# Kernel tuning notes

Measured on AMD Instinct MI355X. Metric: run time of the kernel, lower is better.

Reference implementation:

```python
import jax, jax.numpy as jnp
import numpy as np

NEG_SLOPE = 0.2
EPS = 1e-16


def setup_inputs() -> dict:
    key = jax.random.key(0)
    k1, k2, k3, k4 = jax.random.split(key, 4)
    N, H, F, E = 50000, 4, 32, 800000
    nodes_features = jax.random.normal(k1, (N, H, F), dtype=jnp.float32)
    edge_index = jax.random.randint(k2, (2, E), 0, N, dtype=jnp.int64)
    scoring_fn_source = jax.random.normal(k3, (1, H, F), dtype=jnp.float32)
    scoring_fn_target = jax.random.normal(k4, (1, H, F), dtype=jnp.float32)
    return {
        "nodes_features": nodes_features,
        "scoring_fn_source": scoring_fn_source,
        "scoring_fn_target": scoring_fn_target,
        "edge_index": edge_index,
    }


def reference(nodes_features, scoring_fn_source, scoring_fn_target, edge_index):
    # nodes_features: [N, H, F]; edge_index: [2, E] with row 0 = target, row 1 = source
    num_of_nodes = nodes_features.shape[0]
    trg = edge_index[0]
    src = edge_index[1]

    # Per-node attention logits per head: [N, H]
    scores_source = (nodes_features * scoring_fn_source).sum(axis=-1)
    scores_target = (nodes_features * scoring_fn_target).sum(axis=-1)

    # Lift N -> E via gather: [E, H]
    scores_lifted = scores_source[src] + scores_target[trg]
    src_nodes_features_lifted = nodes_features[src]  # [E, H, F]

    scores_per_edge = jax.nn.leaky_relu(scores_lifted, NEG_SLOPE)
    # Global max subtraction for numerical stability (matches original code)
    scores_per_edge = scores_per_edge - scores_per_edge.max()
    exp_scores = jnp.exp(scores_per_edge)

    # Segment softmax denominator via scatter-add, then gather back per edge
    neighborhood_sums = jax.ops.segment_sum(exp_scores, trg, num_segments=num_of_nodes)
    denom = neighborhood_sums[trg]  # [E, H]

    attentions_per_edge = (exp_scores / (denom + EPS))[..., None]  # [E, H, 1]
    return attentions_per_edge, src_nodes_features_lifted
```

## Files before the change

kernel.cpp:

```cpp
#include <hip/hip_runtime.h>

#define NEG_SLOPE 0.2f
#define EPSV 1e-16f

typedef float f32x4 __attribute__((ext_vector_type(4)));

__device__ __forceinline__ unsigned fenc(float f) {
    unsigned b = __float_as_uint(f);
    return b ^ ((b & 0x80000000u) ? 0xFFFFFFFFu : 0x80000000u);
}
__device__ __forceinline__ float fdec(unsigned u) {
    unsigned b = (u & 0x80000000u) ? (u ^ 0x80000000u) : ~u;
    return __uint_as_float(b);
}
#define FENC_NEG_INF 0x007FFFFFu

__global__ void detect_idx_kernel(const unsigned* __restrict__ ei32,
                                  int* __restrict__ flag) {
    __shared__ int anynz;
    if (threadIdx.x == 0) anynz = 0;
    __syncthreads();
    unsigned v = ei32[2 * threadIdx.x + 1];
    if (v != 0u) anynz = 1;
    __syncthreads();
    if (threadIdx.x == 0) *flag = (anynz ? 0 : 1);
}

__device__ __forceinline__ void load_edge(const void* ei, int is64, int E,
                                          int e, int& trg, int& src) {
    if (is64) {
        const long long* p = (const long long*)ei;
        trg = (int)__builtin_nontemporal_load(&p[e]);
        src = (int)__builtin_nontemporal_load(&p[(size_t)E + e]);
    } else {
        const int* p = (const int*)ei;
        trg = __builtin_nontemporal_load(&p[e]);
        src = __builtin_nontemporal_load(&p[E + e]);
    }
}
__device__ __forceinline__ int load_trg(const void* ei, int is64, int e) {
    if (is64) return (int)__builtin_nontemporal_load(&((const long long*)ei)[e]);
    return __builtin_nontemporal_load(&((const int*)ei)[e]);
}

__global__ void node_scores_kernel(const float* __restrict__ nf,
                                   const float* __restrict__ sfs,
                                   const float* __restrict__ sft,
                                   float* __restrict__ ss,
                                   float* __restrict__ st,
                                   float* __restrict__ nsum,
                                   unsigned* __restrict__ gmax,
                                   int NH) {
    int i = blockIdx.x * blockDim.x + threadIdx.x;
    if (i >= NH) return;
    if (i == 0) *gmax = FENC_NEG_INF;
    int h = i & 3;
    const float4* __restrict__ row = (const float4*)(nf + (size_t)i * 32);
    const float4* __restrict__ as  = (const float4*)(sfs + h * 32);
    const float4* __restrict__ at  = (const float4*)(sft + h * 32);
    float accs = 0.f, acct = 0.f;
#pragma unroll
    for (int q = 0; q < 8; ++q) {
        float4 v = row[q];
        float4 a = as[q];
        float4 b = at[q];
        accs += v.x * a.x + v.y * a.y + v.z * a.z + v.w * a.w;
        acct += v.x * b.x + v.y * b.y + v.z * b.z + v.w * b.w;
    }
    ss[i] = accs;
    st[i] = acct;
    nsum[i] = 0.f;
}


__global__ void edge_lr_max_kernel(const void* __restrict__ ei,
                                   const int* __restrict__ flag,
                                   const float* __restrict__ ss,
                                   const float* __restrict__ st,
                                   float* __restrict__ lrbuf,
                                   unsigned* __restrict__ gmax,
                                   int E) {
    __shared__ float red[256];
    int is64 = *flag;
    int n4 = E * 4;
    int stride = gridDim.x * blockDim.x;
    float lmax = -__builtin_inff();
    for (int i = blockIdx.x * blockDim.x + threadIdx.x; i < n4; i += stride) {
        int e = i >> 2, h = i & 3;
        int trg, src;
        load_edge(ei, is64, E, e, trg, src);
        float s = ss[src * 4 + h] + st[trg * 4 + h];
        float lr = s > 0.f ? s : NEG_SLOPE * s;
        lrbuf[i] = lr;
        lmax = fmaxf(lmax, lr);
    }
    red[threadIdx.x] = lmax;
    __syncthreads();
    for (int off = 128; off > 0; off >>= 1) {
        if (threadIdx.x < off)
            red[threadIdx.x] = fmaxf(red[threadIdx.x], red[threadIdx.x + off]);
        __syncthreads();
    }
    if (threadIdx.x == 0) atomicMax(gmax, fenc(red[0]));
}

__global__ void edge_exp_sum_lean_kernel(const void* __restrict__ ei,
                                         const int* __restrict__ flag,
                                         const unsigned* __restrict__ gmax,
                                         float* __restrict__ lrbuf,
                                         float* __restrict__ nsum,
                                         int E) {
    int is64 = *flag;
    float c = fdec(*gmax);
    int n4 = E * 4;
    int stride = gridDim.x * blockDim.x;
    for (int i = blockIdx.x * blockDim.x + threadIdx.x; i < n4; i += stride) {
        int trg = load_trg(ei, is64, i >> 2);
        float p = __expf(__builtin_nontemporal_load(&lrbuf[i]) - c);
        lrbuf[i] = p;
        atomicAdd(&nsum[trg * 4 + (i & 3)], p);
    }
}

__global__ void att_lean_kernel(const void* __restrict__ ei,
                                const int* __restrict__ flag,
                                const float* __restrict__ pbuf,
                                const float* __restrict__ nsum,
                                float* __restrict__ out,
                                int E) {
    int is64 = *flag;
    int n4 = E * 4;
    int stride = gridDim.x * blockDim.x;
    for (int i = blockIdx.x * blockDim.x + threadIdx.x; i < n4; i += stride) {
        int trg = load_trg(ei, is64, i >> 2);
        float p = __builtin_nontemporal_load(&pbuf[i]);
        float a = p / (nsum[trg * 4 + (i & 3)] + EPSV);
        __builtin_nontemporal_store(a, &out[i]);
    }
}


__device__ __forceinline__ float edge_lr_rc(const void* ei, int is64,
                                            const float* ss, const float* st,
                                            int E, int e, int h, int* trg_out) {
    int trg, src;
    load_edge(ei, is64, E, e, trg, src);
    if (trg_out) *trg_out = trg;
    float s = ss[src * 4 + h] + st[trg * 4 + h];
    return s > 0.f ? s : NEG_SLOPE * s;
}

__global__ void edge_max_fb_kernel(const void* __restrict__ ei,
                                   const int* __restrict__ flag,
                                   const float* __restrict__ ss,
                                   const float* __restrict__ st,
                                   unsigned* __restrict__ gmax, int E) {
    __shared__ float red[256];
    int is64 = *flag;
    int i = blockIdx.x * blockDim.x + threadIdx.x;
    float lr = -__builtin_inff();
    if (i < E * 4) lr = edge_lr_rc(ei, is64, ss, st, E, i >> 2, i & 3, nullptr);
    red[threadIdx.x] = lr;
    __syncthreads();
    for (int off = 128; off > 0; off >>= 1) {
        if (threadIdx.x < off)
            red[threadIdx.x] = fmaxf(red[threadIdx.x], red[threadIdx.x + off]);
        __syncthreads();
    }
    if (threadIdx.x == 0) atomicMax(gmax, fenc(red[0]));
}

__global__ void edge_exp_sum_fb_kernel(const void* __restrict__ ei,
                                       const int* __restrict__ flag,
                                       const float* __restrict__ ss,
                                       const float* __restrict__ st,
                                       const unsigned* __restrict__ gmax,
                                       float* __restrict__ nsum, int E) {
    int i = blockIdx.x * blockDim.x + threadIdx.x;
    if (i >= E * 4) return;
    int is64 = *flag;
    float c = fdec(*gmax);
    int trg;
    float lr = edge_lr_rc(ei, is64, ss, st, E, i >> 2, i & 3, &trg);
    atomicAdd(&nsum[trg * 4 + (i & 3)], __expf(lr - c));
}

__global__ void att_fb_kernel(const void* __restrict__ ei,
                              const int* __restrict__ flag,
                              const float* __restrict__ ss,
                              const float* __restrict__ st,
                              const unsigned* __restrict__ gmax,
                              const float* __restrict__ nsum,
                              float* __restrict__ out, int E) {
    int i = blockIdx.x * blockDim.x + threadIdx.x;
    if (i >= E * 4) return;
    int is64 = *flag;
    float c = fdec(*gmax);
    int trg;
    float lr = edge_lr_rc(ei, is64, ss, st, E, i >> 2, i & 3, &trg);
    float a = __expf(lr - c) / (nsum[trg * 4 + (i & 3)] + EPSV);
    __builtin_nontemporal_store(a, &out[i]);
}

__global__ void gather_feat_kernel(const void* __restrict__ ei,
                                   const int* __restrict__ flag,
                                   const f32x4* __restrict__ nf4,
                                   f32x4* __restrict__ out4,
                                   int E) {
    int is64 = *flag;
    int n = E * 32;
    int stride = gridDim.x * blockDim.x;
    for (int t = blockIdx.x * blockDim.x + threadIdx.x; t < n; t += stride) {
        int e = t >> 5, q = t & 31;
        int src;
        if (is64) {
            src = (int)__builtin_nontemporal_load(&((const long long*)ei)[(size_t)E + e]);
        } else {
            src = __builtin_nontemporal_load(&((const int*)ei)[E + e]);
        }
        f32x4 v = nf4[(size_t)src * 32 + q];
        __builtin_nontemporal_store(v, &out4[(size_t)e * 32 + q]);
    }
}

extern "C" void kernel_launch(void* const* d_in, const int* in_sizes, int n_in,
                              void* d_out, int out_size, void* d_ws, size_t ws_size,
                              hipStream_t stream) {
    const float* nf  = (const float*)d_in[0];
    const float* sfs = (const float*)d_in[1];
    const float* sft = (const float*)d_in[2];
    const void*  ei  = d_in[3];

    const int NH = in_sizes[0] / 32;
    const int E  = in_sizes[3] / 2;

    float* out = (float*)d_out;
    float* ws  = (float*)d_ws;
    float*    ss    = ws;
    float*    st    = ws + NH;
    float*    nsum  = ws + 2 * (size_t)NH;
    int*      flag  = (int*)(ws + 3 * (size_t)NH);
    unsigned* gmax  = (unsigned*)(flag + 1);
    float*    lrbuf = (float*)(gmax + 1);

    size_t need = ((size_t)3 * NH + 2 + (size_t)E * 4) * 4;
    bool lean = ws_size >= need;

    const int B = 256;
    const int n4 = E * 4;

    detect_idx_kernel<<<1, 256, 0, stream>>>((const unsigned*)ei, flag);

    node_scores_kernel<<<(NH + B - 1) / B, B, 0, stream>>>(nf, sfs, sft, ss, st,
                                                           nsum, gmax, NH);

    if (lean) {
        edge_lr_max_kernel<<<2048, B, 0, stream>>>(ei, flag, ss, st, lrbuf, gmax, E);
        edge_exp_sum_lean_kernel<<<2048, B, 0, stream>>>(ei, flag, gmax, lrbuf, nsum, E);
        att_lean_kernel<<<2048, B, 0, stream>>>(ei, flag, lrbuf, nsum, out, E);
    } else {
        edge_max_fb_kernel<<<(n4 + B - 1) / B, B, 0, stream>>>(ei, flag, ss, st, gmax, E);
        edge_exp_sum_fb_kernel<<<(n4 + B - 1) / B, B, 0, stream>>>(ei, flag, ss, st,
                                                                   gmax, nsum, E);
        att_fb_kernel<<<(n4 + B - 1) / B, B, 0, stream>>>(ei, flag, ss, st, gmax,
                                                          nsum, out, E);
    }

    gather_feat_kernel<<<4096, B, 0, stream>>>(
        ei, flag, (const f32x4*)nf, (f32x4*)(out + (size_t)E * 4), E);
}
```

Baseline: 259.3 us.

## Fuse edge max/exp/scatter into one pass with replicated atomic sum buffers

Merges the leaky-relu/max pass and the exp/scatter-add pass into a single per-edge kernel that handles all four heads with vector loads. The global max is applied algebraically in the final normalization, scaling the epsilon by exp(max) instead of subtracting the max before exp. Atomic segment sums go to several replicated buffers chosen by block index, then a fold kernel combines them. This removes one full read/write of the per-edge buffer and reduces atomic contention. The cost is possible overflow of exp without max subtraction for large logits.

```diff
diff --git a/kernel.cpp b/kernel.cpp
--- a/kernel.cpp
+++ b/kernel.cpp
@@ -50,10 +50,11 @@
                                    float* __restrict__ st,
                                    float* __restrict__ nsum,
                                    unsigned* __restrict__ gmax,
-                                   int NH) {
+                                   int NH, int R) {
     int i = blockIdx.x * blockDim.x + threadIdx.x;
     if (i >= NH) return;
     if (i == 0) *gmax = FENC_NEG_INF;
+    for (int r = 0; r < R; ++r) nsum[(size_t)r * NH + i] = 0.f;
     int h = i & 3;
     const float4* __restrict__ row = (const float4*)(nf + (size_t)i * 32);
     const float4* __restrict__ as  = (const float4*)(sfs + h * 32);
@@ -69,30 +70,37 @@
     }
     ss[i] = accs;
     st[i] = acct;
-    nsum[i] = 0.f;
-}
-
-
-__global__ void edge_lr_max_kernel(const void* __restrict__ ei,
-                                   const int* __restrict__ flag,
-                                   const float* __restrict__ ss,
-                                   const float* __restrict__ st,
-                                   float* __restrict__ lrbuf,
-                                   unsigned* __restrict__ gmax,
-                                   int E) {
+}
+
+__global__ void edge_fused_kernel(const void* __restrict__ ei,
+                                  const int* __restrict__ flag,
+                                  const float* __restrict__ ss,
+                                  const float* __restrict__ st,
+                                  float* __restrict__ pbuf,
+                                  float* __restrict__ nsum,
+                                  unsigned* __restrict__ gmax,
+                                  int E, int NH, int R) {
     __shared__ float red[256];
     int is64 = *flag;
-    int n4 = E * 4;
     int stride = gridDim.x * blockDim.x;
+    float* __restrict__ ns = nsum + (size_t)(blockIdx.x & (R - 1)) * NH;
     float lmax = -__builtin_inff();
-    for (int i = blockIdx.x * blockDim.x + threadIdx.x; i < n4; i += stride) {
-        int e = i >> 2, h = i & 3;
+    for (int e = blockIdx.x * blockDim.x + threadIdx.x; e < E; e += stride) {
         int trg, src;
         load_edge(ei, is64, E, e, trg, src);
-        float s = ss[src * 4 + h] + st[trg * 4 + h];
-        float lr = s > 0.f ? s : NEG_SLOPE * s;
-        lrbuf[i] = lr;
-        lmax = fmaxf(lmax, lr);
+        f32x4 a = *(const f32x4*)(ss + (size_t)src * 4);
+        f32x4 b = *(const f32x4*)(st + (size_t)trg * 4);
+        f32x4 s = a + b;
+        f32x4 p;
+#pragma unroll
+        for (int h = 0; h < 4; ++h) {
+            float lr = s[h] > 0.f ? s[h] : NEG_SLOPE * s[h];
+            lmax = fmaxf(lmax, lr);
+            p[h] = __expf(lr);
+        }
+        __builtin_nontemporal_store(p, (f32x4*)(pbuf + (size_t)e * 4));
+#pragma unroll
+        for (int h = 0; h < 4; ++h) atomicAdd(&ns[(size_t)trg * 4 + h], p[h]);
     }
     red[threadIdx.x] = lmax;
     __syncthreads();
@@ -104,41 +112,33 @@
     if (threadIdx.x == 0) atomicMax(gmax, fenc(red[0]));
 }
 
-__global__ void edge_exp_sum_lean_kernel(const void* __restrict__ ei,
-                                         const int* __restrict__ flag,
-                                         const unsigned* __restrict__ gmax,
-                                         float* __restrict__ lrbuf,
-                                         float* __restrict__ nsum,
-                                         int E) {
-    int is64 = *flag;
-    float c = fdec(*gmax);
-    int n4 = E * 4;
-    int stride = gridDim.x * blockDim.x;
-    for (int i = blockIdx.x * blockDim.x + threadIdx.x; i < n4; i += stride) {
-        int trg = load_trg(ei, is64, i >> 2);
-        float p = __expf(__builtin_nontemporal_load(&lrbuf[i]) - c);
-        lrbuf[i] = p;
-        atomicAdd(&nsum[trg * 4 + (i & 3)], p);
-    }
+__global__ void fold_kernel(float* __restrict__ nsum, int N4, int NH, int R) {
+    int i = blockIdx.x * blockDim.x + threadIdx.x;
+    if (i >= N4) return;
+    f32x4 a = ((f32x4*)nsum)[i];
+    for (int r = 1; r < R; ++r)
+        a += *(const f32x4*)(nsum + (size_t)r * NH + (size_t)i * 4);
+    ((f32x4*)nsum)[i] = a;
 }
 
 __global__ void att_lean_kernel(const void* __restrict__ ei,
                                 const int* __restrict__ flag,
                                 const float* __restrict__ pbuf,
                                 const float* __restrict__ nsum,
+                                const unsigned* __restrict__ gmax,
                                 float* __restrict__ out,
                                 int E) {
     int is64 = *flag;
-    int n4 = E * 4;
+    float de = EPSV * __expf(fdec(*gmax));
     int stride = gridDim.x * blockDim.x;
-    for (int i = blockIdx.x * blockDim.x + threadIdx.x; i < n4; i += stride) {
-        int trg = load_trg(ei, is64, i >> 2);
-        float p = __builtin_nontemporal_load(&pbuf[i]);
-        float a = p / (nsum[trg * 4 + (i & 3)] + EPSV);
-        __builtin_nontemporal_store(a, &out[i]);
-    }
-}
-
+    for (int e = blockIdx.x * blockDim.x + threadIdx.x; e < E; e += stride) {
+        int trg = load_trg(ei, is64, e);
+        f32x4 p = __builtin_nontemporal_load((const f32x4*)(pbuf + (size_t)e * 4));
+        f32x4 d = *(const f32x4*)(nsum + (size_t)trg * 4);
+        f32x4 a = p / (d + de);
+        __builtin_nontemporal_store(a, (f32x4*)(out + (size_t)e * 4));
+    }
+}
 
 __device__ __forceinline__ float edge_lr_rc(const void* ei, int is64,
                                             const float* ss, const float* st,
@@ -238,32 +238,41 @@
     float* ws  = (float*)d_ws;
     float*    ss    = ws;
     float*    st    = ws + NH;
-    float*    nsum  = ws + 2 * (size_t)NH;
-    int*      flag  = (int*)(ws + 3 * (size_t)NH);
+    int*      flag  = (int*)(ws + 2 * (size_t)NH);
     unsigned* gmax  = (unsigned*)(flag + 1);
-    float*    lrbuf = (float*)(gmax + 1);
-
-    size_t need = ((size_t)3 * NH + 2 + (size_t)E * 4) * 4;
-    bool lean = ws_size >= need;
+    float*    pbuf  = ws + 2 * (size_t)NH + 4;
+    float*    nsum  = pbuf + (size_t)E * 4;
+
+    int R = 0;
+    for (int r = 8; r >= 1; r >>= 1) {
+        size_t need = ((size_t)2 * NH + 4 + (size_t)E * 4 + (size_t)r * NH) * 4;
+        if (ws_size >= need) { R = r; break; }
+    }
 
     const int B = 256;
-    const int n4 = E * 4;
 
     detect_idx_kernel<<<1, 256, 0, stream>>>((const unsigned*)ei, flag);
 
-    node_scores_kernel<<<(NH + B - 1) / B, B, 0, stream>>>(nf, sfs, sft, ss, st,
-                                                           nsum, gmax, NH);
-
-    if (lean) {
-        edge_lr_max_kernel<<<2048, B, 0, stream>>>(ei, flag, ss, st, lrbuf, gmax, E);
-        edge_exp_sum_lean_kernel<<<2048, B, 0, stream>>>(ei, flag, gmax, lrbuf, nsum, E);
-        att_lean_kernel<<<2048, B, 0, stream>>>(ei, flag, lrbuf, nsum, out, E);
+    if (R > 0) {
+        node_scores_kernel<<<(NH + B - 1) / B, B, 0, stream>>>(nf, sfs, sft, ss, st,
+                                                               nsum, gmax, NH, R);
+        edge_fused_kernel<<<2048, B, 0, stream>>>(ei, flag, ss, st, pbuf, nsum,
+                                                  gmax, E, NH, R);
+        if (R > 1) {
+            int N4 = NH / 4;
+            fold_kernel<<<(N4 + B - 1) / B, B, 0, stream>>>(nsum, N4, NH, R);
+        }
+        att_lean_kernel<<<2048, B, 0, stream>>>(ei, flag, pbuf, nsum, gmax, out, E);
     } else {
+        float* nsum_fb = (float*)(gmax + 1);
+        node_scores_kernel<<<(NH + B - 1) / B, B, 0, stream>>>(nf, sfs, sft, ss, st,
+                                                               nsum_fb, gmax, NH, 1);
+        int n4 = E * 4;
         edge_max_fb_kernel<<<(n4 + B - 1) / B, B, 0, stream>>>(ei, flag, ss, st, gmax, E);
         edge_exp_sum_fb_kernel<<<(n4 + B - 1) / B, B, 0, stream>>>(ei, flag, ss, st,
-                                                                   gmax, nsum, E);
+                                                                   gmax, nsum_fb, E);
         att_fb_kernel<<<(n4 + B - 1) / B, B, 0, stream>>>(ei, flag, ss, st, gmax,
-                                                          nsum, out, E);
+                                                          nsum_fb, out, E);
     }
 
     gather_feat_kernel<<<4096, B, 0, stream>>>(
```

Measured after the change: 349.3 us. +34.7%, slower.

## Fuse max/exp/sum pass and merge attention normalization into feature gather

Applied to the files above, without the earlier changes.

Computes exp of the raw leaky-relu logits in the same pass as the global max and the per-target scatter-add. The max is folded into the denominator epsilon as EPS*exp(max) instead of being subtracted beforehand. Attention normalization is merged into the feature-gather kernel, so the lean path uses two edge kernels instead of four. This removes extra passes over the edge list and the intermediate buffer, but drops the max subtraction and risks exp overflow for large logits.

```diff
diff --git a/kernel.cpp b/kernel.cpp
--- a/kernel.cpp
+++ b/kernel.cpp
@@ -26,21 +26,9 @@
     if (threadIdx.x == 0) *flag = (anynz ? 0 : 1);
 }
 
-__device__ __forceinline__ void load_edge(const void* ei, int is64, int E,
-                                          int e, int& trg, int& src) {
-    if (is64) {
-        const long long* p = (const long long*)ei;
-        trg = (int)__builtin_nontemporal_load(&p[e]);
-        src = (int)__builtin_nontemporal_load(&p[(size_t)E + e]);
-    } else {
-        const int* p = (const int*)ei;
-        trg = __builtin_nontemporal_load(&p[e]);
-        src = __builtin_nontemporal_load(&p[E + e]);
-    }
-}
-__device__ __forceinline__ int load_trg(const void* ei, int is64, int e) {
-    if (is64) return (int)__builtin_nontemporal_load(&((const long long*)ei)[e]);
-    return __builtin_nontemporal_load(&((const int*)ei)[e]);
+__device__ __forceinline__ int load_idx(const void* ei, int is64, size_t k) {
+    if (is64) return (int)__builtin_nontemporal_load(&((const long long*)ei)[k]);
+    return __builtin_nontemporal_load(&((const int*)ei)[k]);
 }
 
 __global__ void node_scores_kernel(const float* __restrict__ nf,
@@ -54,6 +42,7 @@
     int i = blockIdx.x * blockDim.x + threadIdx.x;
     if (i >= NH) return;
     if (i == 0) *gmax = FENC_NEG_INF;
+    nsum[i] = 0.f;
     int h = i & 3;
     const float4* __restrict__ row = (const float4*)(nf + (size_t)i * 32);
     const float4* __restrict__ as  = (const float4*)(sfs + h * 32);
@@ -69,17 +58,16 @@
     }
     ss[i] = accs;
     st[i] = acct;
-    nsum[i] = 0.f;
-}
-
-
-__global__ void edge_lr_max_kernel(const void* __restrict__ ei,
-                                   const int* __restrict__ flag,
-                                   const float* __restrict__ ss,
-                                   const float* __restrict__ st,
-                                   float* __restrict__ lrbuf,
-                                   unsigned* __restrict__ gmax,
-                                   int E) {
+}
+
+__global__ void edge_exp_sum_kernel(const void* __restrict__ ei,
+                                    const int* __restrict__ flag,
+                                    const float* __restrict__ ss,
+                                    const float* __restrict__ st,
+                                    float* __restrict__ pbuf,
+                                    float* __restrict__ nsum,
+                                    unsigned* __restrict__ gmax,
+                                    int E) {
     __shared__ float red[256];
     int is64 = *flag;
     int n4 = E * 4;
@@ -87,12 +75,14 @@
     float lmax = -__builtin_inff();
     for (int i = blockIdx.x * blockDim.x + threadIdx.x; i < n4; i += stride) {
         int e = i >> 2, h = i & 3;
-        int trg, src;
-        load_edge(ei, is64, E, e, trg, src);
+        int trg = load_idx(ei, is64, e);
+        int src = load_idx(ei, is64, (size_t)E + e);
         float s = ss[src * 4 + h] + st[trg * 4 + h];
         float lr = s > 0.f ? s : NEG_SLOPE * s;
-        lrbuf[i] = lr;
         lmax = fmaxf(lmax, lr);
+        float p = __expf(lr);
+        __builtin_nontemporal_store(p, &pbuf[i]);
+        atomicAdd(&nsum[trg * 4 + h], p);
     }
     red[threadIdx.x] = lmax;
     __syncthreads();
@@ -104,63 +94,61 @@
     if (threadIdx.x == 0) atomicMax(gmax, fenc(red[0]));
 }
 
-__global__ void edge_exp_sum_lean_kernel(const void* __restrict__ ei,
-                                         const int* __restrict__ flag,
-                                         const unsigned* __restrict__ gmax,
-                                         float* __restrict__ lrbuf,
-                                         float* __restrict__ nsum,
-                                         int E) {
-    int is64 = *flag;
-    float c = fdec(*gmax);
-    int n4 = E * 4;
-    int stride = gridDim.x * blockDim.x;
-    for (int i = blockIdx.x * blockDim.x + threadIdx.x; i < n4; i += stride) {
-        int trg = load_trg(ei, is64, i >> 2);
-        float p = __expf(__builtin_nontemporal_load(&lrbuf[i]) - c);
-        lrbuf[i] = p;
-        atomicAdd(&nsum[trg * 4 + (i & 3)], p);
-    }
-}
-
-__global__ void att_lean_kernel(const void* __restrict__ ei,
-                                const int* __restrict__ flag,
-                                const float* __restrict__ pbuf,
-                                const float* __restrict__ nsum,
-                                float* __restrict__ out,
-                                int E) {
-    int is64 = *flag;
-    int n4 = E * 4;
-    int stride = gridDim.x * blockDim.x;
-    for (int i = blockIdx.x * blockDim.x + threadIdx.x; i < n4; i += stride) {
-        int trg = load_trg(ei, is64, i >> 2);
-        float p = __builtin_nontemporal_load(&pbuf[i]);
-        float a = p / (nsum[trg * 4 + (i & 3)] + EPSV);
-        __builtin_nontemporal_store(a, &out[i]);
-    }
-}
-
+__global__ void gather_att_kernel(const void* __restrict__ ei,
+                                  const int* __restrict__ flag,
+                                  const f32x4* __restrict__ nf4,
+                                  const float* __restrict__ pbuf,
+                                  const float* __restrict__ nsum,
+                                  const unsigned* __restrict__ gmax,
+                                  float* __restrict__ att_out,
+                                  f32x4* __restrict__ feat_out,
+                                  int E) {
+    int is64 = *flag;
+    float de = EPSV * __expf(fdec(*gmax));
+    int n = E * 32;
+    int stride = gridDim.x * blockDim.x;
+    for (int t = blockIdx.x * blockDim.x + threadIdx.x; t < n; t += stride) {
+        int e = t >> 5, q = t & 31;
+        int src = load_idx(ei, is64, (size_t)E + e);
+        f32x4 v = nf4[(size_t)src * 32 + q];
+        __builtin_nontemporal_store(v, &feat_out[(size_t)e * 32 + q]);
+        if (q < 4) {
+            int trg = load_idx(ei, is64, e);
+            float p = __builtin_nontemporal_load(&pbuf[(size_t)e * 4 + q]);
+            float a = p / (nsum[trg * 4 + q] + de);
+            __builtin_nontemporal_store(a, &att_out[(size_t)e * 4 + q]);
+        }
+    }
+}
 
 __device__ __forceinline__ float edge_lr_rc(const void* ei, int is64,
                                             const float* ss, const float* st,
                                             int E, int e, int h, int* trg_out) {
-    int trg, src;
-    load_edge(ei, is64, E, e, trg, src);
+    int trg = load_idx(ei, is64, e);
+    int src = load_idx(ei, is64, (size_t)E + e);
     if (trg_out) *trg_out = trg;
     float s = ss[src * 4 + h] + st[trg * 4 + h];
     return s > 0.f ? s : NEG_SLOPE * s;
 }
 
-__global__ void edge_max_fb_kernel(const void* __restrict__ ei,
-                                   const int* __restrict__ flag,
-                                   const float* __restrict__ ss,
-                                   const float* __restrict__ st,
-                                   unsigned* __restrict__ gmax, int E) {
+__global__ void edge_exp_sum_fb_kernel(const void* __restrict__ ei,
+                                       const int* __restrict__ flag,
+                                       const float* __restrict__ ss,
+                                       const float* __restrict__ st,
+                                       float* __restrict__ nsum,
+                                       unsigned* __restrict__ gmax, int E) {
     __shared__ float red[256];
     int is64 = *flag;
-    int i = blockIdx.x * blockDim.x + threadIdx.x;
-    float lr = -__builtin_inff();
-    if (i < E * 4) lr = edge_lr_rc(ei, is64, ss, st, E, i >> 2, i & 3, nullptr);
-    red[threadIdx.x] = lr;
+    int n4 = E * 4;
+    int stride = gridDim.x * blockDim.x;
+    float lmax = -__builtin_inff();
+    for (int i = blockIdx.x * blockDim.x + threadIdx.x; i < n4; i += stride) {
+        int trg;
+        float lr = edge_lr_rc(ei, is64, ss, st, E, i >> 2, i & 3, &trg);
+        lmax = fmaxf(lmax, lr);
+        atomicAdd(&nsum[trg * 4 + (i & 3)], __expf(lr));
+    }
+    red[threadIdx.x] = lmax;
     __syncthreads();
     for (int off = 128; off > 0; off >>= 1) {
         if (threadIdx.x < off)
@@ -168,21 +156,6 @@
         __syncthreads();
     }
     if (threadIdx.x == 0) atomicMax(gmax, fenc(red[0]));
-}
-
-__global__ void edge_exp_sum_fb_kernel(const void* __restrict__ ei,
-                                       const int* __restrict__ flag,
-                                       const float* __restrict__ ss,
-                                       const float* __restrict__ st,
-                                       const unsigned* __restrict__ gmax,
-                                       float* __restrict__ nsum, int E) {
-    int i = blockIdx.x * blockDim.x + threadIdx.x;
-    if (i >= E * 4) return;
-    int is64 = *flag;
-    float c = fdec(*gmax);
-    int trg;
-    float lr = edge_lr_rc(ei, is64, ss, st, E, i >> 2, i & 3, &trg);
-    atomicAdd(&nsum[trg * 4 + (i & 3)], __expf(lr - c));
 }
 
 __global__ void att_fb_kernel(const void* __restrict__ ei,
@@ -195,29 +168,23 @@
     int i = blockIdx.x * blockDim.x + threadIdx.x;
     if (i >= E * 4) return;
     int is64 = *flag;
-    float c = fdec(*gmax);
+    float de = EPSV * __expf(fdec(*gmax));
     int trg;
     float lr = edge_lr_rc(ei, is64, ss, st, E, i >> 2, i & 3, &trg);
-    float a = __expf(lr - c) / (nsum[trg * 4 + (i & 3)] + EPSV);
+    float a = __expf(lr) / (nsum[trg * 4 + (i & 3)] + de);
     __builtin_nontemporal_store(a, &out[i]);
 }
 
-__global__ void gather_feat_kernel(const void* __restrict__ ei,
-                                   const int* __restrict__ flag,
-                                   const f32x4* __restrict__ nf4,
-                                   f32x4* __restrict__ out4,
-                                   int E) {
+__global__ void gather_feat_fb_kernel(const void* __restrict__ ei,
+                                      const int* __restrict__ flag,
+                                      const f32x4* __restrict__ nf4,
+                                      f32x4* __restrict__ out4, int E) {
     int is64 = *flag;
     int n = E * 32;
     int stride = gridDim.x * blockDim.x;
     for (int t = blockIdx.x * blockDim.x + threadIdx.x; t < n; t += stride) {
         int e = t >> 5, q = t & 31;
-        int src;
-        if (is64) {
-            src = (int)__builtin_nontemporal_load(&((const long long*)ei)[(size_t)E + e]);
-        } else {
-            src = __builtin_nontemporal_load(&((const int*)ei)[E + e]);
-        }
+        int src = load_idx(ei, is64, (size_t)E + e);
         f32x4 v = nf4[(size_t)src * 32 + q];
         __builtin_nontemporal_store(v, &out4[(size_t)e * 32 + q]);
     }
@@ -241,13 +208,12 @@
     float*    nsum  = ws + 2 * (size_t)NH;
     int*      flag  = (int*)(ws + 3 * (size_t)NH);
     unsigned* gmax  = (unsigned*)(flag + 1);
-    float*    lrbuf = (float*)(gmax + 1);
-
-    size_t need = ((size_t)3 * NH + 2 + (size_t)E * 4) * 4;
+    float*    pbuf  = ws + 3 * (size_t)NH + 4;
+
+    size_t need = ((size_t)3 * NH + 4 + (size_t)E * 4) * 4;
     bool lean = ws_size >= need;
 
     const int B = 256;
-    const int n4 = E * 4;
 
     detect_idx_kernel<<<1, 256, 0, stream>>>((const unsigned*)ei, flag);
 
@@ -255,17 +221,17 @@
                                                            nsum, gmax, NH);
 
     if (lean) {
-        edge_lr_max_kernel<<<2048, B, 0, stream>>>(ei, flag, ss, st, lrbuf, gmax, E);
-        edge_exp_sum_lean_kernel<<<2048, B, 0, stream>>>(ei, flag, gmax, lrbuf, nsum, E);
-        att_lean_kernel<<<2048, B, 0, stream>>>(ei, flag, lrbuf, nsum, out, E);
+        edge_exp_sum_kernel<<<2048, B, 0, stream>>>(ei, flag, ss, st, pbuf,
+                                                    nsum, gmax, E);
+        gather_att_kernel<<<4096, B, 0, stream>>>(ei, flag, (const f32x4*)nf,
+                                                  pbuf, nsum, gmax,
+                                                  out, (f32x4*)(out + (size_t)E * 4), E);
     } else {
-        edge_max_fb_kernel<<<(n4 + B - 1) / B, B, 0, stream>>>(ei, flag, ss, st, gmax, E);
-        edge_exp_sum_fb_kernel<<<(n4 + B - 1) / B, B, 0, stream>>>(ei, flag, ss, st,
-                                                                   gmax, nsum, E);
-        att_fb_kernel<<<(n4 + B - 1) / B, B, 0, stream>>>(ei, flag, ss, st, gmax,
-                                                          nsum, out, E);
-    }
-
-    gather_feat_kernel<<<4096, B, 0, stream>>>(
-        ei, flag, (const f32x4*)nf, (f32x4*)(out + (size_t)E * 4), E);
-}
+        edge_exp_sum_fb_kernel<<<2048, B, 0, stream>>>(ei, flag, ss, st, nsum,
+                                                       gmax, E);
+        att_fb_kernel<<<(E * 4 + B - 1) / B, B, 0, stream>>>(ei, flag, ss, st,
+                                                             gmax, nsum, out, E);
+        gather_feat_fb_kernel<<<4096, B, 0, stream>>>(
+            ei, flag, (const f32x4*)nf, (f32x4*)(out + (size_t)E * 4), E);
+    }
+}
```

Measured after the change: 284.5 us. 9.7% more time.
